# Performance work log

Measured on AMD Instinct MI355X. Metric: run time of the kernel, lower is better.

Reference implementation:

```python
import jax, jax.numpy as jnp
import numpy as np

GRID_SIZE = 5
SPLINE_ORDER = 3
GRID_RANGE = (-1.0, 1.0)
NUM_COEF = GRID_SIZE + SPLINE_ORDER  # 8


def make_grid(in_features):
    h = (GRID_RANGE[1] - GRID_RANGE[0]) / GRID_SIZE
    g = jnp.arange(-SPLINE_ORDER, GRID_SIZE + SPLINE_ORDER + 1, dtype=jnp.float32) * h + GRID_RANGE[0]
    return jnp.broadcast_to(g, (in_features, g.shape[0]))  # (in, grid_size + 2*order + 1)


def b_splines(x, grid):
    # x: (N, in); grid: (in, G). Cox-de Boor recursion -> (N, in, grid_size+order)
    xe = x[..., None]
    bases = ((xe >= grid[:, :-1]) & (xe < grid[:, 1:])).astype(x.dtype)
    for k in range(1, SPLINE_ORDER + 1):
        left = (xe - grid[:, : -(k + 1)]) / (grid[:, k:-1] - grid[:, : -(k + 1)])
        right = (grid[:, k + 1:] - xe) / (grid[:, k + 1:] - grid[:, 1:-k])
        bases = left * bases[..., :-1] + right * bases[..., 1:]
    return bases


def kan_linear(x, grid, base_w, spline_w, scaler):
    # base path: silu(x) @ base_w.T   (base_w: (out, in))
    base_out = jnp.einsum('ni,oi->no', jax.nn.silu(x), base_w)
    # spline path: flatten basis and scaled spline weights into one GEMM
    basis = b_splines(x, grid)                       # (N, in, 8)
    sw = spline_w * scaler[..., None]                # (out, in, 8)
    spline_out = jnp.einsum('nik,oik->no', basis, sw)
    return base_out + spline_out


def setup_inputs() -> dict:
    key = jax.random.key(0)
    ks = jax.random.split(key, 8)
    d = 1024
    dff = 4 * d
    n_tok = 4096
    s = 0.02
    return {
        'x': jax.random.normal(ks[0], (n_tok, d), dtype=jnp.float32),
        'base_w1': jax.random.normal(ks[1], (dff, d), dtype=jnp.float32) * s,
        'spline_w1': jax.random.normal(ks[2], (dff, d, NUM_COEF), dtype=jnp.float32) * s,
        'scaler1': jnp.ones((dff, d), dtype=jnp.float32),
        'base_w2': jax.random.normal(ks[3], (d, dff), dtype=jnp.float32) * s,
        'spline_w2': jax.random.normal(ks[4], (d, dff, NUM_COEF), dtype=jnp.float32) * s,
        'scaler2': jnp.ones((d, dff), dtype=jnp.float32),
        'grid1': make_grid(d),
        'grid2': make_grid(dff),
    }


def reference(x, base_w1, spline_w1, scaler1, base_w2, spline_w2, scaler2, grid1, grid2):
    h = kan_linear(x, grid1, base_w1, spline_w1, scaler1)
    h = jax.nn.gelu(h, approximate=False)  # torch nn.GELU default (erf)
    h = kan_linear(h, grid2, base_w2, spline_w2, scaler2)
    # Dropout(0.1) is identity in eval mode
    return h + x
```

## Files before the change

kernel.cpp:

```cpp
#include <hip/hip_runtime.h>
#include <hip/hip_fp16.h>

typedef _Float16 half_t;
typedef __attribute__((ext_vector_type(8))) _Float16 half8;
typedef __attribute__((ext_vector_type(4))) float f32x4;

#define AS1 __attribute__((address_space(1)))
#define AS3 __attribute__((address_space(3)))

__device__ __forceinline__ void gload16(const half_t* g, half_t* l) {
  __builtin_amdgcn_global_load_lds((const AS1 void*)g, (AS3 void*)l, 16, 0, 0);
}

__device__ __forceinline__ void bspline8u(float x, float out[8]) {
  float g[12];
#pragma unroll
  for (int j = 0; j < 12; ++j) g[j] = (float)(j - 3) * 0.4f - 1.0f;
  float b[11];
#pragma unroll
  for (int j = 0; j < 11; ++j)
    b[j] = (x >= g[j] && x < g[j + 1]) ? 1.0f : 0.0f;
#pragma unroll
  for (int k = 1; k <= 3; ++k) {
#pragma unroll
    for (int j = 0; j + k < 11; ++j) {
      float rl = 1.0f / (g[j + k] - g[j]);
      float rr = 1.0f / (g[j + k + 1] - g[j + 1]);
      b[j] = ((x - g[j]) * rl) * b[j] + ((g[j + k + 1] - x) * rr) * b[j + 1];
    }
  }
#pragma unroll
  for (int j = 0; j < 8; ++j) out[j] = b[j];
}

__global__ void wconv_kernel(const float* __restrict__ bw, const float* __restrict__ sw,
                             const float* __restrict__ sc, half_t* __restrict__ W,
                             int ibits, int ldw) {
  int idx = blockIdx.x * 256 + threadIdx.x;
  int o = idx >> ibits;
  int i = idx & ((1 << ibits) - 1);
  int c = i >> 10;
  int il = i & 1023;
  float b = bw[idx];
  float scv = sc[idx];
  const float4* svp = (const float4*)sw;
  float4 s0 = svp[(size_t)idx * 2];
  float4 s1 = svp[(size_t)idx * 2 + 1];
  half_t* wrow = W + (size_t)o * ldw + c * 9216;
  wrow[il] = (half_t)b;
  half8 hv;
  hv[0] = (half_t)(s0.x * scv); hv[1] = (half_t)(s0.y * scv);
  hv[2] = (half_t)(s0.z * scv); hv[3] = (half_t)(s0.w * scv);
  hv[4] = (half_t)(s1.x * scv); hv[5] = (half_t)(s1.y * scv);
  hv[6] = (half_t)(s1.z * scv); hv[7] = (half_t)(s1.w * scv);
  *(half8*)&wrow[1024 + il * 8] = hv;
}

template <typename ST>
__global__ void expand_kernel(const ST* __restrict__ src, half_t* __restrict__ dst,
                              int Isrc, int i0, int dsub, int kexp) {
  int idx = blockIdx.x * 256 + threadIdx.x;
  int n = idx >> 10;
  int il = idx & 1023;
  float v = (float)src[(size_t)n * Isrc + i0 + il];
  float bs[8];
  bspline8u(v, bs);
  half_t* drow = dst + (size_t)n * kexp + (size_t)dsub * 9216;
  drow[il] = (half_t)(v / (1.0f + expf(-v)));
  half8 hb;
#pragma unroll
  for (int k = 0; k < 8; ++k) hb[k] = (half_t)bs[k];
  *(half8*)&drow[1024 + il * 8] = hb;
}

#define STA(c, t, h)                                                          \
  {                                                                           \
    int r0_ = wid * 8 + (h) * 64;                                             \
    const half_t* g_ = Abase + (size_t)(r0_ + srow) * ldkA +                  \
                       (size_t)(t) * 64 + scol;                               \
    gload16(g_, &As[c][r0_ * 64]);                                            \
    gload16(g_ + (size_t)128 * ldkA, &As[c][(r0_ + 128) * 64]);               \
  }
#define STB(c, t, h)                                                          \
  {                                                                           \
    int r0_ = (wid >> 2) * 64 + (wid & 3) * 8 + (h) * 32;                     \
    const half_t* g_ = Bbase + (size_t)(r0_ + srow) * ldkB +                  \
                       (size_t)(t) * 64 + scol;                               \
    gload16(g_, &Bs[c][r0_ * 64]);                                            \
    gload16(g_ + (size_t)128 * ldkB, &Bs[c][(r0_ + 128) * 64]);               \
  }
#define LOADAF(c, mh)                                                         \
  _Pragma("unroll") for (int a = 0; a < 4; ++a) {                             \
    int row_ = wm * 128 + (mh) * 64 + a * 16 + (lane & 15);                   \
    _Pragma("unroll") for (int ks = 0; ks < 2; ++ks) {                        \
      int ch_ = (ks * 4 + (lane >> 4)) ^ (lane & 7);                          \
      af[a][ks] = *(const half8*)&As[c][row_ * 64 + ch_ * 8];                 \
    }                                                                         \
  }
#define LOADBF(c, nh, bfv)                                                    \
  _Pragma("unroll") for (int b = 0; b < 2; ++b) {                             \
    int row_ = wn * 64 + (nh) * 32 + b * 16 + (lane & 15);                    \
    _Pragma("unroll") for (int ks = 0; ks < 2; ++ks) {                        \
      int ch_ = (ks * 4 + (lane >> 4)) ^ (lane & 7);                          \
      bfv[b][ks] = *(const half8*)&Bs[c][row_ * 64 + ch_ * 8];                \
    }                                                                         \
  }
#define VM6 asm volatile("s_waitcnt vmcnt(6)" ::: "memory");
#define VM0 asm volatile("s_waitcnt vmcnt(0)" ::: "memory");
#define NOVM
#define DOPHASE(mh, nh, bfv, LOADS, STAGE, WAIT)                              \
  do {                                                                        \
    LOADS                                                                     \
    STAGE                                                                     \
    WAIT                                                                      \
    __builtin_amdgcn_s_barrier();                                             \
    __builtin_amdgcn_sched_barrier(0);                                        \
    __builtin_amdgcn_s_setprio(1);                                            \
    _Pragma("unroll") for (int ks = 0; ks < 2; ++ks)                          \
      _Pragma("unroll") for (int a = 0; a < 4; ++a)                           \
        _Pragma("unroll") for (int b = 0; b < 2; ++b)                         \
          acc[(mh) * 4 + a][(nh) * 2 + b] =                                   \
              __builtin_amdgcn_mfma_f32_16x16x32_f16(                         \
                  af[a][ks], bfv[b][ks], acc[(mh) * 4 + a][(nh) * 2 + b],     \
                  0, 0, 0);                                                   \
    __builtin_amdgcn_s_setprio(0);                                            \
    __builtin_amdgcn_s_barrier();                                             \
    __builtin_amdgcn_sched_barrier(0);                                        \
  } while (0)

template <int MODE>
__global__ __launch_bounds__(512, 2) void gemm8_kernel(
    const half_t* __restrict__ A, const half_t* __restrict__ B,
    int ldkA, int ldkB, int kzLen,
    float* __restrict__ Cout, half_t* __restrict__ Hout, int ldc) {
  __shared__ __align__(16) half_t As[2][256 * 64];
  __shared__ __align__(16) half_t Bs[2][256 * 64];

  const int tid = threadIdx.x;
  const int wid = tid >> 6;
  const int lane = tid & 63;
  const int wm = wid >> 2;
  const int wn = wid & 3;

  const half_t* Abase = A + (size_t)blockIdx.x * 256 * ldkA +
                        (size_t)blockIdx.z * kzLen;
  const half_t* Bbase = B + (size_t)blockIdx.y * 256 * ldkB +
                        (size_t)blockIdx.z * kzLen;

  const int srow = lane >> 3;
  const int scol = ((lane & 7) ^ srow) * 8;

  const int nt = kzLen >> 6;

  f32x4 acc[8][4] = {};
  half8 af[4][2], bA[2][2], bB[2][2];

  STA(0, 0, 0); STB(0, 0, 0); STB(0, 0, 1); STA(0, 0, 1);
  STA(1, 1, 0); STB(1, 1, 0); STB(1, 1, 1);
  asm volatile("s_waitcnt vmcnt(0)" ::: "memory");
  __builtin_amdgcn_s_barrier();
  __builtin_amdgcn_sched_barrier(0);

  for (int i = 0; i < (nt >> 1) - 1; ++i) {
    const int t = 2 * i;
    DOPHASE(0, 0, bA, { LOADAF(0, 0) LOADBF(0, 0, bA) }, { STA(1, t + 1, 1); }, NOVM);
    DOPHASE(0, 1, bB, { LOADBF(0, 1, bB) },              { STA(0, t + 2, 0); }, NOVM);
    DOPHASE(1, 1, bB, { LOADAF(0, 1) },                  { STB(0, t + 2, 0); }, NOVM);
    DOPHASE(1, 0, bA, {},                                { STB(0, t + 2, 1); }, VM6);
    DOPHASE(0, 0, bA, { LOADAF(1, 0) LOADBF(1, 0, bA) }, { STA(0, t + 2, 1); }, NOVM);
    DOPHASE(0, 1, bB, { LOADBF(1, 1, bB) },              { STA(1, t + 3, 0); }, NOVM);
    DOPHASE(1, 1, bB, { LOADAF(1, 1) },                  { STB(1, t + 3, 0); }, NOVM);
    DOPHASE(1, 0, bA, {},                                { STB(1, t + 3, 1); }, VM6);
  }
  {
    const int t = nt - 2;
    DOPHASE(0, 0, bA, { LOADAF(0, 0) LOADBF(0, 0, bA) }, { STA(1, t + 1, 1); }, NOVM);
    DOPHASE(0, 1, bB, { LOADBF(0, 1, bB) },              {},                   NOVM);
    DOPHASE(1, 1, bB, { LOADAF(0, 1) },                  {},                   NOVM);
    DOPHASE(1, 0, bA, {},                                {},                   VM0);
    DOPHASE(0, 0, bA, { LOADAF(1, 0) LOADBF(1, 0, bA) }, {},                   NOVM);
    DOPHASE(0, 1, bB, { LOADBF(1, 1, bB) },              {},                   NOVM);
    DOPHASE(1, 1, bB, { LOADAF(1, 1) },                  {},                   NOVM);
    DOPHASE(1, 0, bA, {},                                {},                   NOVM);
  }

  const int r_lo = (lane >> 4) << 2;
  const int col0 = (int)blockIdx.y * 256 + wn * 64 + (lane & 15);
  const int row00 = (int)blockIdx.x * 256 + wm * 128 + r_lo;
#pragma unroll
  for (int mf = 0; mf < 8; ++mf)
#pragma unroll
    for (int nf = 0; nf < 4; ++nf)
#pragma unroll
      for (int j = 0; j < 4; ++j) {
        float v = acc[mf][nf][j];
        size_t off = (size_t)(row00 + mf * 16 + j) * ldc + col0 + nf * 16;
        if constexpr (MODE == 0) {
          v = 0.5f * v * (1.0f + erff(v * 0.70710678118654752f));
          Hout[off] = (half_t)v;
        } else {
          atomicAdd(&Cout[off], v);
        }
      }
}

extern "C" void kernel_launch(void* const* d_in, const int* in_sizes, int n_in,
                              void* d_out, int out_size, void* d_ws, size_t ws_size,
                              hipStream_t stream) {
  const float* x   = (const float*)d_in[0];
  const float* bw1 = (const float*)d_in[1];
  const float* sw1 = (const float*)d_in[2];
  const float* sc1 = (const float*)d_in[3];
  const float* bw2 = (const float*)d_in[4];
  const float* sw2 = (const float*)d_in[5];
  const float* sc2 = (const float*)d_in[6];
  float* out = (float*)d_out;

  half_t* Wbuf = (half_t*)d_ws;
  const size_t W_HALVES = (size_t)4096 * 9216;
  const size_t A1_HALVES = (size_t)4096 * 9216;
  const size_t HH_HALVES = (size_t)4096 * 4096;
  int abuf_chunks = 1;
  if (ws_size >= (W_HALVES + A1_HALVES * 4 + HH_HALVES) * sizeof(half_t))
    abuf_chunks = 4;
  else if (ws_size >= (W_HALVES + A1_HALVES * 2 + HH_HALVES) * sizeof(half_t))
    abuf_chunks = 2;
  half_t* Abuf = Wbuf + W_HALVES;
  half_t* Hh   = Abuf + A1_HALVES * abuf_chunks;

  const int T = 256;
  const int NB = (4096 * 1024) / T;

  hipMemcpyAsync(out, x, (size_t)4096 * 1024 * sizeof(float),
                 hipMemcpyDeviceToDevice, stream);

  wconv_kernel<<<NB, T, 0, stream>>>(bw1, sw1, sc1, Wbuf, 10, 9216);
  expand_kernel<float><<<NB, T, 0, stream>>>(x, Abuf, 1024, 0, 0, 9216);
  gemm8_kernel<0><<<dim3(16, 16, 1), 512, 0, stream>>>(
      Abuf, Wbuf, 9216, 9216, 9216, nullptr, Hh, 4096);

  wconv_kernel<<<NB, T, 0, stream>>>(bw2, sw2, sc2, Wbuf, 12, 36864);
  if (abuf_chunks == 4) {
    for (int c = 0; c < 4; ++c)
      expand_kernel<half_t><<<NB, T, 0, stream>>>(Hh, Abuf, 4096, c * 1024, c, 36864);
    gemm8_kernel<4><<<dim3(16, 4, 4), 512, 0, stream>>>(
        Abuf, Wbuf, 36864, 36864, 9216, out, nullptr, 1024);
  } else if (abuf_chunks == 2) {
    for (int c = 0; c < 2; ++c) {
      expand_kernel<half_t><<<NB, T, 0, stream>>>(Hh, Abuf, 4096, c * 2048, 0, 18432);
      expand_kernel<half_t><<<NB, T, 0, stream>>>(Hh, Abuf, 4096, c * 2048 + 1024, 1, 18432);
      gemm8_kernel<4><<<dim3(16, 4, 4), 512, 0, stream>>>(
          Abuf, Wbuf + (size_t)c * 18432, 18432, 36864, 4608, out, nullptr, 1024);
    }
  } else {
    for (int c = 0; c < 4; ++c) {
      expand_kernel<half_t><<<NB, T, 0, stream>>>(Hh, Abuf, 4096, c * 1024, 0, 9216);
      gemm8_kernel<4><<<dim3(16, 4, 4), 512, 0, stream>>>(
          Abuf, Wbuf + (size_t)c * 9216, 9216, 36864, 2304, out, nullptr, 1024);
    }
  }
}
```

Measured before the change: 898.0 us.

## Prefetch next-phase B fragments into double-buffered registers and reschedule stores

Splits the B-fragment register buffer into even/odd copies so the next stage's B fragment loads from LDS during the current phase's MFMAs instead of at phase start. It also reorders the global-to-LDS stores across the eight phases and changes the vmcnt waits to VM6 on every phase. The goal is to hide LDS read latency and spread global loads more evenly. The cost is extra VGPRs, which could lower occupancy or cause spills, and more frequent vmcnt waits.

```diff
diff --git a/kernel.cpp b/kernel.cpp
--- a/kernel.cpp
+++ b/kernel.cpp
@@ -153,35 +153,36 @@
   const int nt = kzLen >> 6;
 
   f32x4 acc[8][4] = {};
-  half8 af[4][2], bA[2][2], bB[2][2];
+  half8 af[4][2], bAe[2][2], bAo[2][2], bB[2][2];
 
   STA(0, 0, 0); STB(0, 0, 0); STB(0, 0, 1); STA(0, 0, 1);
-  STA(1, 1, 0); STB(1, 1, 0); STB(1, 1, 1);
+  STA(1, 1, 0); STB(1, 1, 0);
   asm volatile("s_waitcnt vmcnt(0)" ::: "memory");
   __builtin_amdgcn_s_barrier();
   __builtin_amdgcn_sched_barrier(0);
+  LOADBF(0, 0, bAe)
 
   for (int i = 0; i < (nt >> 1) - 1; ++i) {
     const int t = 2 * i;
-    DOPHASE(0, 0, bA, { LOADAF(0, 0) LOADBF(0, 0, bA) }, { STA(1, t + 1, 1); }, NOVM);
-    DOPHASE(0, 1, bB, { LOADBF(0, 1, bB) },              { STA(0, t + 2, 0); }, NOVM);
-    DOPHASE(1, 1, bB, { LOADAF(0, 1) },                  { STB(0, t + 2, 0); }, NOVM);
-    DOPHASE(1, 0, bA, {},                                { STB(0, t + 2, 1); }, VM6);
-    DOPHASE(0, 0, bA, { LOADAF(1, 0) LOADBF(1, 0, bA) }, { STA(0, t + 2, 1); }, NOVM);
-    DOPHASE(0, 1, bB, { LOADBF(1, 1, bB) },              { STA(1, t + 3, 0); }, NOVM);
-    DOPHASE(1, 1, bB, { LOADAF(1, 1) },                  { STB(1, t + 3, 0); }, NOVM);
-    DOPHASE(1, 0, bA, {},                                { STB(1, t + 3, 1); }, VM6);
+    DOPHASE(0, 0, bAe, { LOADAF(0, 0) },      { STB(1, t + 1, 1); }, VM6);
+    DOPHASE(0, 1, bB,  { LOADBF(0, 1, bB) },  { STA(1, t + 1, 1); }, VM6);
+    DOPHASE(1, 1, bB,  { LOADAF(0, 1) },      { STA(0, t + 2, 0); }, VM6);
+    DOPHASE(1, 0, bAe, { LOADBF(1, 0, bAo) }, { STB(0, t + 2, 0); }, VM6);
+    DOPHASE(0, 0, bAo, { LOADAF(1, 0) },      { STB(0, t + 2, 1); }, VM6);
+    DOPHASE(0, 1, bB,  { LOADBF(1, 1, bB) },  { STA(0, t + 2, 1); }, VM6);
+    DOPHASE(1, 1, bB,  { LOADAF(1, 1) },      { STA(1, t + 3, 0); }, VM6);
+    DOPHASE(1, 0, bAo, { LOADBF(0, 0, bAe) }, { STB(1, t + 3, 0); }, VM6);
   }
   {
     const int t = nt - 2;
-    DOPHASE(0, 0, bA, { LOADAF(0, 0) LOADBF(0, 0, bA) }, { STA(1, t + 1, 1); }, NOVM);
-    DOPHASE(0, 1, bB, { LOADBF(0, 1, bB) },              {},                   NOVM);
-    DOPHASE(1, 1, bB, { LOADAF(0, 1) },                  {},                   NOVM);
-    DOPHASE(1, 0, bA, {},                                {},                   VM0);
-    DOPHASE(0, 0, bA, { LOADAF(1, 0) LOADBF(1, 0, bA) }, {},                   NOVM);
-    DOPHASE(0, 1, bB, { LOADBF(1, 1, bB) },              {},                   NOVM);
-    DOPHASE(1, 1, bB, { LOADAF(1, 1) },                  {},                   NOVM);
-    DOPHASE(1, 0, bA, {},                                {},                   NOVM);
+    DOPHASE(0, 0, bAe, { LOADAF(0, 0) },      { STB(1, t + 1, 1); }, VM6);
+    DOPHASE(0, 1, bB,  { LOADBF(0, 1, bB) },  { STA(1, t + 1, 1); }, VM6);
+    DOPHASE(1, 1, bB,  { LOADAF(0, 1) },      {},                   VM0);
+    DOPHASE(1, 0, bAe, { LOADBF(1, 0, bAo) }, {},                   NOVM);
+    DOPHASE(0, 0, bAo, { LOADAF(1, 0) },      {},                   NOVM);
+    DOPHASE(0, 1, bB,  { LOADBF(1, 1, bB) },  {},                   NOVM);
+    DOPHASE(1, 1, bB,  { LOADAF(1, 1) },      {},                   NOVM);
+    DOPHASE(1, 0, bAo, {},                    {},                   NOVM);
   }
 
   const int r_lo = (lane >> 4) << 2;
```

After: 859.6 us. -4.3%, faster.
